# Optimization experiments

Hardware: AMD Instinct MI355X
Metric: run time of the kernel (lower is better)

The kernel has to match this reference:

```python
import jax, jax.numpy as jnp
import numpy as np

SCALE = 10.0

def _transform_point_cloud(xyz, T_src, T_tgt, H, W):
    # xyz: [B,3,H,W] -> [B,3,H,W] transformed into target camera frame
    B = xyz.shape[0]
    xyzh = jnp.concatenate([xyz.reshape(B, 3, -1), jnp.ones((B, 1, H * W), xyz.dtype)], axis=1)
    M = jnp.linalg.inv(T_tgt) @ T_src  # [4,4]
    out = jnp.einsum('ij,bjn->bin', M, xyzh)[:, :3]
    return out.reshape(B, 3, H, W)

def _project_point_cloud(xyz, feat, K, H, W):
    # xyz: [B,3,H,W], feat: [B,C1,H,W], K: [3,3]. Default flips: horizontal=0, vertical=1.
    B, C1 = feat.shape[0], feat.shape[1]
    xyz = xyz.reshape(B, 3, -1)
    z = xyz[:, 2:3, :]
    im = jnp.round(jnp.einsum('ij,bjn->bin', K, xyz / z))  # [B,3,N]
    x, y = im[:, 0, :], im[:, 1, :]
    valid = (x > 0) & (x < W) & (y > 0) & (y < H)
    # invalid points scatter into dummy slot H*W which is sliced off
    idx = jnp.where(valid, y * W + x, float(H * W)).astype(jnp.int32)  # [B,N]
    ff = feat.reshape(B, C1, -1)
    def scat(f, i):  # f: [C1,N], i: [N]
        return jnp.zeros((C1, H * W + 1), f.dtype).at[:, i].set(f)[:, :H * W]
    dst = jax.vmap(scat)(ff, idx).reshape(B, C1, H, W)
    return dst[:, :, ::-1, :]  # flip vertically (default flip_vertically=1)

def reference(feature, xyzi, T, CAM_MTX, unet_w, unet_b, label):
    B, CAM, C, H, W = feature.shape
    z = xyzi[:, :, 2, :, :]  # [B,CAM,H,W]
    soft = []
    for t in range(CAM):
        feats = []
        for s in range(CAM):
            fs = jnp.concatenate([feature[:, s], z[:, s][:, None]], axis=1)  # [B,C+1,H,W]
            if s != t:
                xyz_t = _transform_point_cloud(xyzi[:, s, :3], T[s], T[t], H, W)
                fs = _project_point_cloud(xyz_t, fs, CAM_MTX[t], H, W)
            feats.append(fs)
        # deterministic stand-in for torch.randperm ordering: target first, rest ascending
        order = [t] + [s for s in range(CAM) if s != t]
        fap = jnp.stack([feats[s] for s in order], axis=1) / SCALE  # [B,CAM,C+1,H,W]
        x = fap.reshape(B, CAM * (C + 1), H, W)
        # UNet stand-in (UNet undefined in source): 1x1 conv (C+1)*CAM -> C
        soft.append(jnp.einsum('oc,bchw->bohw', unet_w, x) + unet_b[None, :, None, None])
    return (jnp.stack(soft, axis=1), label)

def setup_inputs() -> dict:
    key = jax.random.key(0)
    ks = jax.random.split(key, 6)
    B, CAM, C, H, W = 2, 4, 14, 480, 640
    feature = jax.random.normal(ks[0], (B, CAM, C, H, W), jnp.float32)
    zc = jax.random.uniform(ks[1], (B, CAM, 1, H, W), jnp.float32, 1.0, 4.0)
    xy = (jax.random.uniform(ks[2], (B, CAM, 2, H, W), jnp.float32) - 0.5) * 1.2 * zc
    inten = jax.random.uniform(ks[3], (B, CAM, 1, H, W), jnp.float32)
    xyzi = jnp.concatenate([xy, zc, inten], axis=2)
    label = jax.random.randint(ks[4], (B, CAM, H, W), 0, C, jnp.int64)
    Tm = np.tile(np.eye(4, dtype=np.float32), (CAM, 1, 1))
    for k in range(CAM):
        Tm[k, 0, 3] = 0.05 * k
        Tm[k, 1, 3] = -0.03 * k
    K = np.tile(np.array([[500.0, 0.0, W / 2.0], [0.0, 500.0, H / 2.0], [0.0, 0.0, 1.0]], np.float32), (CAM, 1, 1))
    unet_w = jax.random.normal(ks[5], (C, (C + 1) * CAM), jnp.float32) * 0.05
    unet_b = jnp.zeros((C,), jnp.float32)
    return {"feature": feature, "xyzi": xyzi, "T": jnp.asarray(Tm), "CAM_MTX": jnp.asarray(K), "unet_w": unet_w, "unet_b": unet_b, "label": label}
```

## Files before the change

### kernel.cpp

```cpp
#include <hip/hip_runtime.h>

constexpr int B    = 2;
constexpr int CAM  = 4;
constexpr int C    = 14;
constexpr int H    = 480;
constexpr int W    = 640;
constexpr int NPIX = H * W;
constexpr int PK   = 16;

constexpr int SROWS  = 8;
constexpr int STRIPS = H / SROWS;
constexpr int SCELL  = SROWS * W;
constexpr int CAP    = 6144;
constexpr int NSLICE = B * CAM * 3;

constexpr int ABLK     = 1024;
constexpr int IPT      = 4;
constexpr int BPB      = ABLK * IPT;
constexpr int NBIN_BLK = NPIX / BPB;
constexpr int BIN_BLKS = NSLICE * NBIN_BLK;
constexpr int NPACK_BLK= NPIX / ABLK;
constexpr int PACK_BLKS= B * CAM * NPACK_BLK;
constexpr int LAB_BLKS = B * CAM * NPIX / 4 / ABLK;
static_assert(NPIX % BPB == 0, "bin tiling");

__global__ void compute_M_kernel(const float* __restrict__ T,
                                 float* __restrict__ Mout) {
    const int id = threadIdx.x;
    if (blockIdx.x != 0 || id >= CAM * CAM) return;
    const int t = id / CAM;
    const int s = id - t * CAM;
    float A[4][8];
    for (int i = 0; i < 4; ++i)
        for (int j = 0; j < 4; ++j) {
            A[i][j]     = T[t * 16 + i * 4 + j];
            A[i][4 + j] = (i == j) ? 1.f : 0.f;
        }
    for (int col = 0; col < 4; ++col) {
        int piv = col;
        for (int r = col + 1; r < 4; ++r)
            if (fabsf(A[r][col]) > fabsf(A[piv][col])) piv = r;
        if (piv != col)
            for (int j = 0; j < 8; ++j) {
                float tmp = A[col][j]; A[col][j] = A[piv][j]; A[piv][j] = tmp;
            }
        float d = A[col][col];
        for (int j = 0; j < 8; ++j) A[col][j] /= d;
        for (int r = 0; r < 4; ++r) {
            if (r == col) continue;
            float m = A[r][col];
            for (int j = 0; j < 8; ++j) A[r][j] -= m * A[col][j];
        }
    }
    for (int i = 0; i < 3; ++i)
        for (int j = 0; j < 4; ++j) {
            float acc = 0.f;
            for (int k = 0; k < 4; ++k)
                acc += A[i][4 + k] * T[s * 16 + k * 4 + j];
            Mout[(t * CAM + s) * 12 + i * 4 + j] = acc;
        }
}

__device__ __forceinline__ bool project_xyz(float x, float y, float z,
                                            const float* __restrict__ Mp,
                                            const float* __restrict__ Kp,
                                            int& strip, int& tloc) {
    const float xt = __fadd_rn(__fadd_rn(__fadd_rn(__fmul_rn(Mp[0], x),
                      __fmul_rn(Mp[1], y)), __fmul_rn(Mp[2], z)), Mp[3]);
    const float yt = __fadd_rn(__fadd_rn(__fadd_rn(__fmul_rn(Mp[4], x),
                      __fmul_rn(Mp[5], y)), __fmul_rn(Mp[6], z)), Mp[7]);
    const float zt = __fadd_rn(__fadd_rn(__fadd_rn(__fmul_rn(Mp[8], x),
                      __fmul_rn(Mp[9], y)), __fmul_rn(Mp[10], z)), Mp[11]);

    const float vx = __fdiv_rn(xt, zt);
    const float vy = __fdiv_rn(yt, zt);
    const float u = __fadd_rn(__fadd_rn(__fmul_rn(Kp[0], vx),
                      __fmul_rn(Kp[1], vy)), Kp[2]);
    const float v = __fadd_rn(__fadd_rn(__fmul_rn(Kp[3], vx),
                      __fmul_rn(Kp[4], vy)), Kp[5]);

    const float ur = rintf(u);
    const float vr = rintf(v);

    if (ur > 0.f && ur < (float)W && vr > 0.f && vr < (float)H) {
        const int iv = (int)vr, iu = (int)ur;
        strip = iv >> 3;
        tloc  = (iv & (SROWS - 1)) * W + iu;
        return true;
    }
    return false;
}

__device__ __forceinline__ bool project(const float* __restrict__ xyzi,
                                        const float* __restrict__ Mp,
                                        const float* __restrict__ Kp,
                                        int bs, int n, int& strip, int& tloc) {
    const float* src = xyzi + (size_t)bs * 4 * NPIX;
    return project_xyz(src[n], src[NPIX + n], src[2 * NPIX + n],
                       Mp, Kp, strip, tloc);
}

__global__ __launch_bounds__(ABLK) void phaseA_kernel(
        const float* __restrict__ xyzi, const float* __restrict__ feature,
        const float* __restrict__ M, const float* __restrict__ Kmtx,
        const int* __restrict__ lab, unsigned int* __restrict__ bins,
        int* __restrict__ gcount, float* __restrict__ packed,
        float* __restrict__ outLab) {
    __shared__ int cnt[STRIPS];
    __shared__ int gbase[STRIPS];
    const int bid = blockIdx.x;
    const int tid = threadIdx.x;

    if (bid < BIN_BLKS) {
        const int slice = bid / NBIN_BLK;
        const int base  = (bid - slice * NBIN_BLK) * BPB;
        const int b = slice / 12;
        const int r = slice - b * 12;
        const int t = r / 3;
        const int j = r - t * 3;
        const int s = j + (j >= t ? 1 : 0);
        const float* __restrict__ Mp = M + (t * CAM + s) * 12;
        const float* __restrict__ Kp = Kmtx + t * 9;
        const float* __restrict__ src = xyzi + (size_t)(b * CAM + s) * 4 * NPIX;

        if (tid < STRIPS) cnt[tid] = 0;
        __syncthreads();

        float xv[IPT], yv[IPT], zv[IPT];
#pragma unroll
        for (int k = 0; k < IPT; ++k) {
            const int n = base + k * ABLK + tid;
            xv[k] = src[n];
            yv[k] = src[NPIX + n];
            zv[k] = src[2 * NPIX + n];
        }

        bool valid[IPT];
        int strip[IPT], tloc[IPT], lslot[IPT];
#pragma unroll
        for (int k = 0; k < IPT; ++k) {
            strip[k] = 0; tloc[k] = 0; lslot[k] = 0;
            valid[k] = project_xyz(xv[k], yv[k], zv[k], Mp, Kp,
                                   strip[k], tloc[k]);
            if (valid[k]) lslot[k] = atomicAdd(&cnt[strip[k]], 1);
        }
        __syncthreads();
        if (tid < STRIPS && cnt[tid] > 0)
            gbase[tid] = atomicAdd(&gcount[slice * STRIPS + tid], cnt[tid]);
        __syncthreads();
#pragma unroll
        for (int k = 0; k < IPT; ++k) {
            if (valid[k]) {
                const int pos = gbase[strip[k]] + lslot[k];
                if (pos < CAP)
                    bins[((size_t)(slice * STRIPS + strip[k])) * CAP + pos] =
                        ((unsigned int)tloc[k] << 19) |
                        (unsigned int)(base + k * ABLK + tid);
            }
        }
    } else if (bid < BIN_BLKS + PACK_BLKS) {
        const int q  = bid - BIN_BLKS;
        const int bs = q / NPACK_BLK;
        const int n  = (q - bs * NPACK_BLK) * ABLK + tid;
        const float* fb = feature + (size_t)bs * C * NPIX + n;
        float* pb = packed + ((size_t)bs * NPIX + n) * PK;
        float v[PK];
#pragma unroll
        for (int c = 0; c < C; ++c)
            v[c] = __fdiv_rn(fb[(size_t)c * NPIX], 10.0f);
        v[14] = __fdiv_rn(xyzi[((size_t)bs * 4 + 2) * NPIX + n], 10.0f);
        v[15] = 0.f;
#pragma unroll
        for (int q4 = 0; q4 < 4; ++q4)
            *(float4*)(pb + q4 * 4) =
                make_float4(v[q4*4], v[q4*4+1], v[q4*4+2], v[q4*4+3]);
    } else {
        const int q = bid - (BIN_BLKS + PACK_BLKS);
        const int i = q * ABLK + tid;
        const int4 l4 = ((const int4*)lab)[i];
        ((float4*)outLab)[i] = make_float4((float)l4.x, (float)l4.y,
                                           (float)l4.z, (float)l4.w);
    }
}

__global__ __launch_bounds__(256) void phaseB_kernel(
        const unsigned int* __restrict__ bins, const int* __restrict__ gcount,
        int* __restrict__ winner) {
    __shared__ int tile[SCELL];
    const int bid = blockIdx.x;
    for (int i = threadIdx.x; i < SCELL; i += 256) tile[i] = -1;
    __syncthreads();
    int cntv = gcount[bid];
    if (cntv > CAP) cntv = CAP;
    const unsigned int* bp = bins + (size_t)bid * CAP;
    for (int i = threadIdx.x; i < cntv; i += 256) {
        const unsigned int e = bp[i];
        atomicMax(&tile[e >> 19], (int)(e & 0x7FFFFu));
    }
    __syncthreads();
    const int slice = bid / STRIPS;
    const int strip = bid - slice * STRIPS;
    int* wp = winner + (size_t)slice * NPIX + strip * SCELL;
    for (int i = threadIdx.x; i < SCELL; i += 256) wp[i] = tile[i];
}

__global__ __launch_bounds__(256) void fuse_kernel(
        const float* __restrict__ packed, const int* __restrict__ winner,
        const float* __restrict__ Wmat, const float* __restrict__ bias,
        float* __restrict__ out) {
    __shared__ float sW[C * 60];
    __shared__ float sB[C];
    for (int i = threadIdx.x; i < C * 60; i += 256) sW[i] = Wmat[i];
    if (threadIdx.x < C) sB[threadIdx.x] = bias[threadIdx.x];
    __syncthreads();

    const int n  = blockIdx.x * 256 + threadIdx.x;
    const int bt = blockIdx.y;
    const int b  = bt / CAM;
    const int t  = bt - b * CAM;
    const int h  = n / W;
    const int w  = n - h * W;
    const int pFlip = (H - 1 - h) * W + w;

    float acc[C];
#pragma unroll
    for (int o = 0; o < C; ++o) acc[o] = 0.f;

#pragma unroll
    for (int g = 0; g < CAM; ++g) {
        int s, pix;
        if (g == 0) {
            s = t; pix = n;
        } else {
            const int j = g - 1;
            s = j + (j >= t ? 1 : 0);
            const int wn = winner[(size_t)(b * 12 + t * 3 + j) * NPIX + pFlip];
            if (wn < 0) continue;
            pix = wn;
        }
        const float* pb = packed + ((size_t)(b * CAM + s) * NPIX + pix) * PK;
        float v[PK];
#pragma unroll
        for (int q = 0; q < 4; ++q) {
            const float4 f4 = *(const float4*)(pb + q * 4);
            v[q*4] = f4.x; v[q*4+1] = f4.y; v[q*4+2] = f4.z; v[q*4+3] = f4.w;
        }
#pragma unroll
        for (int c = 0; c < 15; ++c) {
#pragma unroll
            for (int o = 0; o < C; ++o)
                acc[o] = __fadd_rn(acc[o], __fmul_rn(sW[o * 60 + g * 15 + c], v[c]));
        }
    }

    float* ob = out + (size_t)bt * C * NPIX + n;
#pragma unroll
    for (int o = 0; o < C; ++o)
        ob[(size_t)o * NPIX] = __fadd_rn(acc[o], sB[o]);
}

__global__ __launch_bounds__(256) void winner_kernel(
        const float* __restrict__ xyzi, const float* __restrict__ M,
        const float* __restrict__ Kmtx, int* __restrict__ winner) {
    const int n    = blockIdx.x * 256 + threadIdx.x;
    const int pair = blockIdx.y;
    const int b = pair / 12;
    const int r = pair - b * 12;
    const int t = r / 3;
    const int j = r - t * 3;
    const int s = j + (j >= t ? 1 : 0);
    int strip, tloc;
    if (project(xyzi, M + (t * CAM + s) * 12, Kmtx + t * 9,
                b * CAM + s, n, strip, tloc)) {
        const int idx = strip * SCELL + tloc;
        atomicMax(&winner[(size_t)pair * NPIX + idx], n);
    }
}

__global__ __launch_bounds__(256) void pack_kernel(
        const float* __restrict__ feature, const float* __restrict__ xyzi,
        float* __restrict__ packed) {
    const int n  = blockIdx.x * 256 + threadIdx.x;
    const int bs = blockIdx.y;
    const float* fb = feature + (size_t)bs * C * NPIX + n;
    float* pb = packed + ((size_t)bs * NPIX + n) * PK;
    float v[PK];
#pragma unroll
    for (int c = 0; c < C; ++c)
        v[c] = __fdiv_rn(fb[(size_t)c * NPIX], 10.0f);
    v[14] = __fdiv_rn(xyzi[((size_t)bs * 4 + 2) * NPIX + n], 10.0f);
    v[15] = 0.f;
#pragma unroll
    for (int q = 0; q < 4; ++q)
        *(float4*)(pb + q * 4) = make_float4(v[q*4], v[q*4+1], v[q*4+2], v[q*4+3]);
}

__global__ __launch_bounds__(256) void fuse_fallback_kernel(
        const float* __restrict__ feature, const float* __restrict__ xyzi,
        const int* __restrict__ winner, const float* __restrict__ Wmat,
        const float* __restrict__ bias, float* __restrict__ out) {
    __shared__ float sW[C * 60];
    __shared__ float sB[C];
    for (int i = threadIdx.x; i < C * 60; i += 256) sW[i] = Wmat[i];
    if (threadIdx.x < C) sB[threadIdx.x] = bias[threadIdx.x];
    __syncthreads();
    const int n  = blockIdx.x * 256 + threadIdx.x;
    const int bt = blockIdx.y;
    const int b  = bt / CAM;
    const int t  = bt - b * CAM;
    const int h  = n / W;
    const int w  = n - h * W;
    const int pFlip = (H - 1 - h) * W + w;
    float acc[C];
#pragma unroll
    for (int o = 0; o < C; ++o) acc[o] = 0.f;
#pragma unroll
    for (int g = 0; g < CAM; ++g) {
        int s, pix;
        if (g == 0) { s = t; pix = n; }
        else {
            const int j = g - 1;
            s = j + (j >= t ? 1 : 0);
            const int wn = winner[(size_t)(b * 12 + t * 3 + j) * NPIX + pFlip];
            if (wn < 0) continue;
            pix = wn;
        }
        const float* fb = feature + (size_t)(b * CAM + s) * C * NPIX + pix;
        const float zv  = xyzi[((size_t)(b * CAM + s) * 4 + 2) * NPIX + pix];
#pragma unroll
        for (int c = 0; c < C; ++c) {
            const float xc = __fdiv_rn(fb[(size_t)c * NPIX], 10.0f);
#pragma unroll
            for (int o = 0; o < C; ++o)
                acc[o] = __fadd_rn(acc[o], __fmul_rn(sW[o * 60 + g * 15 + c], xc));
        }
        const float zc = __fdiv_rn(zv, 10.0f);
#pragma unroll
        for (int o = 0; o < C; ++o)
            acc[o] = __fadd_rn(acc[o], __fmul_rn(sW[o * 60 + g * 15 + 14], zc));
    }
    float* ob = out + (size_t)bt * C * NPIX + n;
#pragma unroll
    for (int o = 0; o < C; ++o)
        ob[(size_t)o * NPIX] = __fadd_rn(acc[o], sB[o]);
}

__global__ __launch_bounds__(256) void label_copy_kernel(
        const int* __restrict__ lab, float* __restrict__ out) {
    const int i = blockIdx.x * 256 + threadIdx.x;
    const int4 l4 = ((const int4*)lab)[i];
    ((float4*)out)[i] = make_float4((float)l4.x, (float)l4.y,
                                    (float)l4.z, (float)l4.w);
}

extern "C" void kernel_launch(void* const* d_in, const int* in_sizes, int n_in,
                              void* d_out, int out_size, void* d_ws, size_t ws_size,
                              hipStream_t stream) {
    const float* feature = (const float*)d_in[0];
    const float* xyzi    = (const float*)d_in[1];
    const float* T       = (const float*)d_in[2];
    const float* Kmtx    = (const float*)d_in[3];
    const float* unet_w  = (const float*)d_in[4];
    const float* unet_b  = (const float*)d_in[5];
    const int*   label   = (const int*)d_in[6];
    float* out = (float*)d_out;
    float* outLab = out + (size_t)B * CAM * C * NPIX;

    const size_t winnerBytes = (size_t)NSLICE * NPIX * sizeof(int);
    const size_t gcountBytes = (size_t)NSLICE * STRIPS * sizeof(int);
    const size_t binsBytes   = (size_t)NSLICE * STRIPS * CAP * sizeof(unsigned int);
    const size_t packedBytes = (size_t)B * CAM * NPIX * PK * sizeof(float);
    const size_t fastBytes   = winnerBytes + gcountBytes + binsBytes + packedBytes + 1024;

    if (ws_size >= fastBytes) {
        int*          winner = (int*)d_ws;
        int*          gcount = (int*)((char*)d_ws + winnerBytes);
        unsigned int* bins   = (unsigned int*)((char*)d_ws + winnerBytes + gcountBytes);
        float*        packed = (float*)((char*)d_ws + winnerBytes + gcountBytes + binsBytes);
        float*        Mbuf   = (float*)((char*)d_ws + winnerBytes + gcountBytes + binsBytes + packedBytes);

        hipMemsetAsync(gcount, 0, gcountBytes, stream);
        compute_M_kernel<<<1, 64, 0, stream>>>(T, Mbuf);

        const int gA = BIN_BLKS + PACK_BLKS + LAB_BLKS;
        phaseA_kernel<<<gA, ABLK, 0, stream>>>(xyzi, feature, Mbuf, Kmtx,
                                               label, bins, gcount, packed, outLab);
        phaseB_kernel<<<NSLICE * STRIPS, 256, 0, stream>>>(bins, gcount, winner);

        dim3 g2(NPIX / 256, B * CAM);
        fuse_kernel<<<g2, 256, 0, stream>>>(packed, winner, unet_w, unet_b, out);
    } else {
        int*   winner = (int*)d_ws;
        float* packed = (float*)((char*)d_ws + winnerBytes);
        float* Mbuf   = (float*)((char*)d_ws + winnerBytes + packedBytes);
        const bool havePacked = ws_size >= winnerBytes + packedBytes + 256;
        if (!havePacked) Mbuf = (float*)((char*)d_ws + winnerBytes);

        hipMemsetAsync(winner, 0xFF, winnerBytes, stream);
        compute_M_kernel<<<1, 64, 0, stream>>>(T, Mbuf);

        dim3 g1(NPIX / 256, NSLICE);
        winner_kernel<<<g1, 256, 0, stream>>>(xyzi, Mbuf, Kmtx, winner);

        dim3 g2(NPIX / 256, B * CAM);
        if (havePacked) {
            pack_kernel<<<g2, 256, 0, stream>>>(feature, xyzi, packed);
            fuse_kernel<<<g2, 256, 0, stream>>>(packed, winner, unet_w, unet_b, out);
        } else {
            fuse_fallback_kernel<<<g2, 256, 0, stream>>>(feature, xyzi, winner,
                                                         unet_w, unet_b, out);
        }
        label_copy_kernel<<<B * CAM * NPIX / 4 / 256, 256, 0, stream>>>(label, outLab);
    }
}
```

Measured before the change: 492.1 us.

## Hoist all gather loads ahead of compute in fuse kernel and use FMA

The fuse kernel now issues all three winner-index loads and all four 64-byte packed-feature gathers up front, before the 1x1-conv accumulation. Previously the loads were interleaved with the math, so each camera's gather was serialized. Invalid winners get zeroed vectors instead of a skipped iteration. Separate mul+add is replaced by fused FMA, and launch bounds now request four blocks per CU. In exchange the kernel holds 64 extra live floats in registers, which may raise register pressure or cause spills under the occupancy hint. The FMA changes rounding relative to the reference's separate multiply and add.

New measurement: 475.5 us. 1.03x faster.

```diff
diff --git a/kernel.cpp b/kernel.cpp
--- a/kernel.cpp
+++ b/kernel.cpp
@@ -204,7 +204,7 @@
     for (int i = threadIdx.x; i < SCELL; i += 256) wp[i] = tile[i];
 }
 
-__global__ __launch_bounds__(256) void fuse_kernel(
+__global__ __launch_bounds__(256, 4) void fuse_kernel(
         const float* __restrict__ packed, const int* __restrict__ winner,
         const float* __restrict__ Wmat, const float* __restrict__ bias,
         float* __restrict__ out) {
@@ -222,34 +222,48 @@
     const int w  = n - h * W;
     const int pFlip = (H - 1 - h) * W + w;
 
-    float acc[C];
-#pragma unroll
-    for (int o = 0; o < C; ++o) acc[o] = 0.f;
-
-#pragma unroll
-    for (int g = 0; g < CAM; ++g) {
-        int s, pix;
-        if (g == 0) {
-            s = t; pix = n;
-        } else {
-            const int j = g - 1;
-            s = j + (j >= t ? 1 : 0);
-            const int wn = winner[(size_t)(b * 12 + t * 3 + j) * NPIX + pFlip];
-            if (wn < 0) continue;
-            pix = wn;
-        }
-        const float* pb = packed + ((size_t)(b * CAM + s) * NPIX + pix) * PK;
-        float v[PK];
+    int wn[3];
+#pragma unroll
+    for (int j = 0; j < 3; ++j)
+        wn[j] = winner[(size_t)(b * 12 + t * 3 + j) * NPIX + pFlip];
+
+    float v[4][16];
+    {
+        const float* pb = packed + ((size_t)(b * CAM + t) * NPIX + n) * PK;
 #pragma unroll
         for (int q = 0; q < 4; ++q) {
             const float4 f4 = *(const float4*)(pb + q * 4);
-            v[q*4] = f4.x; v[q*4+1] = f4.y; v[q*4+2] = f4.z; v[q*4+3] = f4.w;
-        }
+            v[0][q*4] = f4.x; v[0][q*4+1] = f4.y;
+            v[0][q*4+2] = f4.z; v[0][q*4+3] = f4.w;
+        }
+    }
+#pragma unroll
+    for (int j = 0; j < 3; ++j) {
+        const int s = j + (j >= t ? 1 : 0);
+        if (wn[j] >= 0) {
+            const float* pb = packed + ((size_t)(b * CAM + s) * NPIX + wn[j]) * PK;
+#pragma unroll
+            for (int q = 0; q < 4; ++q) {
+                const float4 f4 = *(const float4*)(pb + q * 4);
+                v[j+1][q*4] = f4.x; v[j+1][q*4+1] = f4.y;
+                v[j+1][q*4+2] = f4.z; v[j+1][q*4+3] = f4.w;
+            }
+        } else {
+#pragma unroll
+            for (int q = 0; q < 16; ++q) v[j+1][q] = 0.f;
+        }
+    }
+
+    float acc[C];
+#pragma unroll
+    for (int o = 0; o < C; ++o) acc[o] = 0.f;
+#pragma unroll
+    for (int g = 0; g < CAM; ++g) {
 #pragma unroll
         for (int c = 0; c < 15; ++c) {
 #pragma unroll
             for (int o = 0; o < C; ++o)
-                acc[o] = __fadd_rn(acc[o], __fmul_rn(sW[o * 60 + g * 15 + c], v[c]));
+                acc[o] = __builtin_fmaf(sW[o * 60 + g * 15 + c], v[g][c], acc[o]);
         }
     }
 
```
